# Optimization experiments

Hardware: AMD Instinct MI355X
Metric: run time of the kernel (lower is better)

The kernel has to match this reference:

```python
import jax, jax.numpy as jnp
import numpy as np

B, S, H = 2, 2048, 1024
NH, G = 16, 4
HD = H // NH          # 64
HPG = NH // G         # 4 heads per kv group


def _xavier(key, fan_in, fan_out):
    limit = np.sqrt(6.0 / (fan_in + fan_out)).astype(np.float32)
    return jax.random.uniform(key, (fan_in, fan_out), jnp.float32, -limit, limit)


def setup_inputs() -> dict:
    key = jax.random.key(0)
    ks = jax.random.split(key, 6)
    hidden_state = jax.random.normal(ks[0], (B, S, H), jnp.float32)
    causal = jnp.tril(jnp.ones((S, S), dtype=bool))
    attention_mask = jnp.broadcast_to(causal, (B, NH, S, S))
    # weights stored as (in, out); torch nn.Linear computes x @ W.T, equivalent math
    Wq = _xavier(ks[1], H, H)
    Wk = _xavier(ks[2], H, G * HD)
    Wv = _xavier(ks[3], H, G * HD)
    Wo = _xavier(ks[4], H, H)
    bq = jnp.zeros((H,), jnp.float32)
    bk = jnp.zeros((G * HD,), jnp.float32)
    bv = jnp.zeros((G * HD,), jnp.float32)
    bo = jnp.zeros((H,), jnp.float32)
    return {"hidden_state": hidden_state, "attention_mask": attention_mask,
            "Wq": Wq, "bq": bq, "Wk": Wk, "bk": bk,
            "Wv": Wv, "bv": bv, "Wo": Wo, "bo": bo}


def reference(hidden_state, attention_mask, Wq, bq, Wk, bk, Wv, bv, Wo, bo):
    b, s, _ = hidden_state.shape
    scale = jnp.float32(1.0 / np.sqrt(HD))
    # projections; query heads split as (group, head_in_group) = head-major order
    q = (hidden_state @ Wq + bq).reshape(b, s, G, HPG, HD)
    k = (hidden_state @ Wk + bk).reshape(b, s, G, HD)
    v = (hidden_state @ Wv + bv).reshape(b, s, G, HD)
    # scores: [b, G, HPG, S, S]  (kv broadcast over heads_per_group, as in torch expand)
    scores = jnp.einsum('bqghd,bkgd->bghqk', q, k) * scale
    mask = attention_mask.reshape(b, G, HPG, s, s)
    scores = jnp.where(mask, scores, -jnp.inf)
    w = jax.nn.softmax(scores, axis=-1)  # dropout=0 (eval): identity
    out = jnp.einsum('bghqk,bkgd->bqghd', w, v).reshape(b, s, H)
    return out @ Wo + bo
```

## Files before the change

### kernel.cpp

```cpp
#include <hip/hip_runtime.h>

#define BATCH 2
#define SEQ   2048
#define HDIM  1024
#define NHEAD 16
#define NGRP  4
#define HDHD  64
#define QKVN  1536
#define MROWS (BATCH*SEQ)

#define DI __device__ __forceinline__

typedef __attribute__((ext_vector_type(4))) float f32x4;
typedef __attribute__((ext_vector_type(8))) __bf16 bf16x8;
typedef __attribute__((ext_vector_type(8))) unsigned short ushort8;

DI unsigned short f2bf(float f) {
    unsigned int u = __float_as_uint(f);
    u += 0x7FFF + ((u >> 16) & 1);
    return (unsigned short)(u >> 16);
}

DI void async16(const void* g, void* l) {
    __builtin_amdgcn_global_load_lds(
        (const __attribute__((address_space(1))) unsigned int*)g,
        (__attribute__((address_space(3))) unsigned int*)l, 16, 0, 0);
}

#define MFMA16(a, b, c) __builtin_amdgcn_mfma_f32_16x16x32_bf16((a), (b), (c), 0, 0, 0)

__global__ __launch_bounds__(256) void cvt_bf16_kernel(
    const float* __restrict__ in, unsigned short* __restrict__ out, int n8)
{
    int i = blockIdx.x * 256 + threadIdx.x;
    if (i >= n8) return;
    const float4* p = (const float4*)in;
    float4 a = p[i * 2];
    float4 b = p[i * 2 + 1];
    ushort8 r;
    r[0] = f2bf(a.x); r[1] = f2bf(a.y); r[2] = f2bf(a.z); r[3] = f2bf(a.w);
    r[4] = f2bf(b.x); r[5] = f2bf(b.y); r[6] = f2bf(b.z); r[7] = f2bf(b.w);
    *(ushort8*)&out[i * 8] = r;
}

__global__ __launch_bounds__(256) void wtrans_kernel(
    const float* __restrict__ W, unsigned short* __restrict__ Wt, int K, int N)
{
    __shared__ float t[32][33];
    int k0 = blockIdx.y * 32, n0 = blockIdx.x * 32;
    int tx = threadIdx.x & 31, ty = threadIdx.x >> 5;
#pragma unroll
    for (int i = 0; i < 4; ++i)
        t[ty + i * 8][tx] = W[(size_t)(k0 + ty + i * 8) * N + n0 + tx];
    __syncthreads();
#pragma unroll
    for (int i = 0; i < 4; ++i)
        Wt[(size_t)(n0 + ty + i * 8) * K + k0 + tx] = f2bf(t[tx][ty + i * 8]);
}

__global__ void biascat_kernel(const float* __restrict__ bq,
                               const float* __restrict__ bk,
                               const float* __restrict__ bv,
                               float* __restrict__ out)
{
    int i = blockIdx.x * 256 + threadIdx.x;
    if (i < 1024)      out[i] = bq[i];
    else if (i < 1280) out[i] = bk[i - 1024];
    else if (i < 1536) out[i] = bv[i - 1280];
}

template<bool BF16_OUT>
__global__ __launch_bounds__(256) void gemm_bt(
    const unsigned short* __restrict__ A,
    const unsigned short* __restrict__ Bt,
    const float* __restrict__ bias,
    void* __restrict__ C,
    int M, int N, int K, int ldc)
{
    __shared__ unsigned short Asm[128 * 64];
    __shared__ unsigned short Bsm[128 * 64];
    const int tid = threadIdx.x;
    const int lane = tid & 63;
    const int w = tid >> 6;
    const int l15 = lane & 15;
    const int l4  = lane >> 4;
    const int m0 = blockIdx.y * 128;
    const int n0 = blockIdx.x * 128;
    const int wm = (w >> 1) * 64;
    const int wn = (w & 1) * 64;

    f32x4 acc[4][4] = {};

    const int srow = tid >> 3;
    const int c8   = (tid & 7) * 8;

    for (int kb = 0; kb < K; kb += 64) {
#pragma unroll
        for (int i = 0; i < 4; ++i) {
            int r = srow + i * 32;
            async16(&A[(size_t)(m0 + r) * K + kb + c8], &Asm[r * 64 + c8]);
        }
#pragma unroll
        for (int i = 0; i < 4; ++i) {
            int r = srow + i * 32;
            async16(&Bt[(size_t)(n0 + r) * K + kb + c8], &Bsm[r * 64 + c8]);
        }
        __syncthreads();
#pragma unroll
        for (int kk = 0; kk < 2; ++kk) {
            bf16x8 a[4], b[4];
#pragma unroll
            for (int mi = 0; mi < 4; ++mi)
                a[mi] = *(const bf16x8*)&Asm[(wm + mi * 16 + l15) * 64 + kk * 32 + l4 * 8];
#pragma unroll
            for (int ni = 0; ni < 4; ++ni)
                b[ni] = *(const bf16x8*)&Bsm[(wn + ni * 16 + l15) * 64 + kk * 32 + l4 * 8];
#pragma unroll
            for (int mi = 0; mi < 4; ++mi)
#pragma unroll
                for (int ni = 0; ni < 4; ++ni)
                    acc[mi][ni] = MFMA16(a[mi], b[ni], acc[mi][ni]);
        }
        __syncthreads();
    }

#pragma unroll
    for (int ni = 0; ni < 4; ++ni) {
        int n = n0 + wn + ni * 16 + l15;
        float bv = bias[n];
#pragma unroll
        for (int mi = 0; mi < 4; ++mi) {
            int mrow = m0 + wm + mi * 16 + l4 * 4;
#pragma unroll
            for (int r = 0; r < 4; ++r) {
                float v = acc[mi][ni][r] + bv;
                if (BF16_OUT)
                    ((unsigned short*)C)[(size_t)(mrow + r) * ldc + n] = f2bf(v);
                else
                    ((float*)C)[(size_t)(mrow + r) * ldc + n] = v;
            }
        }
    }
}

__global__ __launch_bounds__(256) void vtrans_kernel(
    const unsigned short* __restrict__ QKV, unsigned short* __restrict__ Vt)
{
    int bg = blockIdx.y;
    int s0 = blockIdx.x * 64;
    int b = bg >> 2, g = bg & 3;
    int t = threadIdx.x;
    int sr = t >> 3;
    int dc = (t & 7) * 8;
#pragma unroll
    for (int p = 0; p < 2; ++p) {
        int s = s0 + sr + p * 32;
        ushort8 v = *(const ushort8*)&QKV[(size_t)(b * SEQ + s) * QKVN + 1280 + g * 64 + dc];
#pragma unroll
        for (int j = 0; j < 8; ++j)
            Vt[((size_t)bg * 64 + dc + j) * SEQ + s] = v[j];
    }
}

__global__ __launch_bounds__(256) void flash_gqa(
    const unsigned short* __restrict__ QKV,
    const unsigned short* __restrict__ Vt,
    unsigned short* __restrict__ O)
{
    const int tid  = threadIdx.x;
    const int lane = tid & 63;
    const int w    = tid >> 6;
    const int l15  = lane & 15;
    const int l4   = lane >> 4;
    const int qb   = blockIdx.x;
    const int h    = blockIdx.y;
    const int b    = blockIdx.z;
    const int g    = h >> 2;
    const int q0   = qb * 64 + w * 16;

    __shared__ unsigned short Pl[4][16 * 72];
    unsigned short* P = &Pl[w][0];

    const unsigned short* Qb = QKV + (size_t)(b * SEQ) * QKVN + h * 64;
    const unsigned short* Kb = QKV + (size_t)(b * SEQ) * QKVN + 1024 + g * 64;
    const unsigned short* Vb = Vt + ((size_t)(b * NGRP + g) * 64) * SEQ;

    bf16x8 qa[2];
#pragma unroll
    for (int ks = 0; ks < 2; ++ks)
        qa[ks] = *(const bf16x8*)&Qb[(size_t)(q0 + l15) * QKVN + ks * 32 + l4 * 8];

    f32x4 acc[4] = {};
    float m[4], ssum[4];
#pragma unroll
    for (int r = 0; r < 4; ++r) { m[r] = -1e30f; ssum[r] = 0.f; }

    const float scale = 0.125f;
    const int nkt = qb + 1;

    for (int kt = 0; kt < nkt; ++kt) {
        const int kbase = kt * 64;
        f32x4 st[4];
#pragma unroll
        for (int n = 0; n < 4; ++n) {
            f32x4 s4 = {0.f, 0.f, 0.f, 0.f};
#pragma unroll
            for (int ks = 0; ks < 2; ++ks) {
                bf16x8 kf = *(const bf16x8*)&Kb[(size_t)(kbase + n * 16 + l15) * QKVN + ks * 32 + l4 * 8];
                s4 = MFMA16(qa[ks], kf, s4);
            }
            st[n] = s4;
        }
        const bool diag = (kbase + 63 > q0);
#pragma unroll
        for (int n = 0; n < 4; ++n)
#pragma unroll
            for (int r = 0; r < 4; ++r) {
                float v = st[n][r] * scale;
                if (diag) {
                    int key = kbase + n * 16 + l15;
                    int q   = q0 + l4 * 4 + r;
                    if (key > q) v = -1e30f;
                }
                st[n][r] = v;
            }
        float tm[4];
#pragma unroll
        for (int r = 0; r < 4; ++r)
            tm[r] = fmaxf(fmaxf(st[0][r], st[1][r]), fmaxf(st[2][r], st[3][r]));
#pragma unroll
        for (int msk = 1; msk < 16; msk <<= 1)
#pragma unroll
            for (int r = 0; r < 4; ++r)
                tm[r] = fmaxf(tm[r], __shfl_xor(tm[r], msk, 64));
        float fr[4];
#pragma unroll
        for (int r = 0; r < 4; ++r) {
            float mn = fmaxf(m[r], tm[r]);
            fr[r] = __expf(m[r] - mn);
            m[r] = mn;
        }
        float rs[4] = {0.f, 0.f, 0.f, 0.f};
#pragma unroll
        for (int n = 0; n < 4; ++n)
#pragma unroll
            for (int r = 0; r < 4; ++r) {
                float p = __expf(st[n][r] - m[r]);
                st[n][r] = p;
                rs[r] += p;
            }
#pragma unroll
        for (int msk = 1; msk < 16; msk <<= 1)
#pragma unroll
            for (int r = 0; r < 4; ++r)
                rs[r] += __shfl_xor(rs[r], msk, 64);
#pragma unroll
        for (int r = 0; r < 4; ++r) ssum[r] = ssum[r] * fr[r] + rs[r];
#pragma unroll
        for (int n = 0; n < 4; ++n)
#pragma unroll
            for (int r = 0; r < 4; ++r) acc[n][r] *= fr[r];
#pragma unroll
        for (int n = 0; n < 4; ++n)
#pragma unroll
            for (int r = 0; r < 4; ++r)
                P[(l4 * 4 + r) * 72 + n * 16 + l15] = f2bf(st[n][r]);
        __syncthreads();
#pragma unroll
        for (int n = 0; n < 4; ++n) {
#pragma unroll
            for (int ks = 0; ks < 2; ++ks) {
                bf16x8 pa = *(const bf16x8*)&P[l15 * 72 + ks * 32 + l4 * 8];
                bf16x8 vb = *(const bf16x8*)&Vb[(size_t)(n * 16 + l15) * SEQ + kbase + ks * 32 + l4 * 8];
                acc[n] = MFMA16(pa, vb, acc[n]);
            }
        }
        __syncthreads();
    }

    float inv[4];
#pragma unroll
    for (int r = 0; r < 4; ++r) inv[r] = 1.f / ssum[r];
#pragma unroll
    for (int n = 0; n < 4; ++n)
#pragma unroll
        for (int r = 0; r < 4; ++r) {
            float v = acc[n][r] * inv[r];
            O[(size_t)(b * SEQ + q0 + l4 * 4 + r) * HDIM + h * 64 + n * 16 + l15] = f2bf(v);
        }
}

extern "C" void kernel_launch(void* const* d_in, const int* in_sizes, int n_in,
                              void* d_out, int out_size, void* d_ws, size_t ws_size,
                              hipStream_t stream)
{
    const float* hidden = (const float*)d_in[0];
    const float* Wq = (const float*)d_in[2];
    const float* bq = (const float*)d_in[3];
    const float* Wk = (const float*)d_in[4];
    const float* bk = (const float*)d_in[5];
    const float* Wv = (const float*)d_in[6];
    const float* bv = (const float*)d_in[7];
    const float* Wo = (const float*)d_in[8];
    const float* bo = (const float*)d_in[9];

    char* ws = (char*)d_ws;
    unsigned short* Xb      = (unsigned short*)(ws);
    unsigned short* QKV     = (unsigned short*)(ws + 8388608);
    unsigned short* WqkvT   = (unsigned short*)(ws + 20971520);
    unsigned short* WoT     = (unsigned short*)(ws + 24117248);
    unsigned short* Vt      = (unsigned short*)(ws + 26214400);
    unsigned short* AttnOut = (unsigned short*)(ws + 30408704);
    float*          bqkv    = (float*)(ws + 38797312);

    cvt_bf16_kernel<<<dim3((MROWS * HDIM) / 8 / 256), 256, 0, stream>>>(hidden, Xb, (MROWS * HDIM) / 8);

    wtrans_kernel<<<dim3(32, 32), 256, 0, stream>>>(Wq, WqkvT,                  HDIM, 1024);
    wtrans_kernel<<<dim3( 8, 32), 256, 0, stream>>>(Wk, WqkvT + 1024 * HDIM,    HDIM,  256);
    wtrans_kernel<<<dim3( 8, 32), 256, 0, stream>>>(Wv, WqkvT + 1280 * HDIM,    HDIM,  256);
    wtrans_kernel<<<dim3(32, 32), 256, 0, stream>>>(Wo, WoT,                    HDIM, 1024);

    biascat_kernel<<<dim3(6), 256, 0, stream>>>(bq, bk, bv, bqkv);

    gemm_bt<true><<<dim3(QKVN / 128, MROWS / 128), 256, 0, stream>>>(
        Xb, WqkvT, bqkv, QKV, MROWS, QKVN, HDIM, QKVN);

    vtrans_kernel<<<dim3(SEQ / 64, BATCH * NGRP), 256, 0, stream>>>(QKV, Vt);

    flash_gqa<<<dim3(SEQ / 64, NHEAD, BATCH), 256, 0, stream>>>(QKV, Vt, AttnOut);

    gemm_bt<false><<<dim3(HDIM / 128, MROWS / 128), 256, 0, stream>>>(
        AttnOut, WoT, bo, (float*)d_out, MROWS, HDIM, HDIM, HDIM);
}
```

Measured before the change: 944.6 us.

## Pre-pack K/V into MFMA fragment layouts in QKV GEMM epilogue; drop LDS P staging

The QKV GEMM epilogue now writes K and V directly into fragment-packed layouts, so the separate V transpose kernel is no longer needed and flash attention reads K and V with contiguous 16-byte loads instead of strided row reads. The attention kernel computes S transposed (K as the A operand), which lets the exponentiated probabilities be packed straight into bf16 A fragments for the PV MFMA without the shared-memory round trip and the two block barriers per tile. It also folds the scale into an exp2 constant and computes row sums with an MFMA against a ones vector instead of shuffle reductions. The cost is more complex scattered epilogue stores in the projection GEMM and an extra cross-lane shuffle to broadcast the rescale factors.

```diff
diff --git a/kernel.cpp b/kernel.cpp
--- a/kernel.cpp
+++ b/kernel.cpp
@@ -5,7 +5,6 @@
 #define HDIM  1024
 #define NHEAD 16
 #define NGRP  4
-#define HDHD  64
 #define QKVN  1536
 #define MROWS (BATCH*SEQ)
 
@@ -14,12 +13,15 @@
 typedef __attribute__((ext_vector_type(4))) float f32x4;
 typedef __attribute__((ext_vector_type(8))) __bf16 bf16x8;
 typedef __attribute__((ext_vector_type(8))) unsigned short ushort8;
+typedef __attribute__((ext_vector_type(4))) unsigned short us4;
 
 DI unsigned short f2bf(float f) {
     unsigned int u = __float_as_uint(f);
     u += 0x7FFF + ((u >> 16) & 1);
     return (unsigned short)(u >> 16);
 }
+
+DI bf16x8 u2b(ushort8 u) { union { ushort8 u; bf16x8 b; } x; x.u = u; return x.b; }
 
 DI void async16(const void* g, void* l) {
     __builtin_amdgcn_global_load_lds(
@@ -69,12 +71,14 @@
     else if (i < 1536) out[i] = bv[i - 1280];
 }
 
-template<bool BF16_OUT>
+template<int MODE>
 __global__ __launch_bounds__(256) void gemm_bt(
     const unsigned short* __restrict__ A,
     const unsigned short* __restrict__ Bt,
     const float* __restrict__ bias,
     void* __restrict__ C,
+    unsigned short* __restrict__ Kp,
+    unsigned short* __restrict__ Vp,
     int M, int N, int K, int ldc)
 {
     __shared__ unsigned short Asm[128 * 64];
@@ -124,47 +128,70 @@
         __syncthreads();
     }
 
-#pragma unroll
-    for (int ni = 0; ni < 4; ++ni) {
-        int n = n0 + wn + ni * 16 + l15;
-        float bv = bias[n];
-#pragma unroll
-        for (int mi = 0; mi < 4; ++mi) {
-            int mrow = m0 + wm + mi * 16 + l4 * 4;
-#pragma unroll
-            for (int r = 0; r < 4; ++r) {
-                float v = acc[mi][ni][r] + bv;
-                if (BF16_OUT)
-                    ((unsigned short*)C)[(size_t)(mrow + r) * ldc + n] = f2bf(v);
-                else
-                    ((float*)C)[(size_t)(mrow + r) * ldc + n] = v;
-            }
-        }
-    }
-}
-
-__global__ __launch_bounds__(256) void vtrans_kernel(
-    const unsigned short* __restrict__ QKV, unsigned short* __restrict__ Vt)
-{
-    int bg = blockIdx.y;
-    int s0 = blockIdx.x * 64;
-    int b = bg >> 2, g = bg & 3;
-    int t = threadIdx.x;
-    int sr = t >> 3;
-    int dc = (t & 7) * 8;
-#pragma unroll
-    for (int p = 0; p < 2; ++p) {
-        int s = s0 + sr + p * 32;
-        ushort8 v = *(const ushort8*)&QKV[(size_t)(b * SEQ + s) * QKVN + 1280 + g * 64 + dc];
-#pragma unroll
-        for (int j = 0; j < 8; ++j)
-            Vt[((size_t)bg * 64 + dc + j) * SEQ + s] = v[j];
+    if (MODE == 0) {
+#pragma unroll
+        for (int ni = 0; ni < 4; ++ni) {
+            int n = n0 + wn + ni * 16 + l15;
+            float bv = bias[n];
+#pragma unroll
+            for (int mi = 0; mi < 4; ++mi) {
+                int mrow = m0 + wm + mi * 16 + l4 * 4;
+#pragma unroll
+                for (int r = 0; r < 4; ++r)
+                    ((float*)C)[(size_t)(mrow + r) * ldc + n] = acc[mi][ni][r] + bv;
+            }
+        }
+    } else {
+        const int bidx = m0 >> 11;
+#pragma unroll
+        for (int ni = 0; ni < 4; ++ni) {
+            const int nb = n0 + wn + ni * 16;
+            const float bv = bias[nb + l15];
+            if (nb < 1024) {
+#pragma unroll
+                for (int mi = 0; mi < 4; ++mi) {
+                    int mrow = m0 + wm + mi * 16 + l4 * 4;
+#pragma unroll
+                    for (int r = 0; r < 4; ++r)
+                        ((unsigned short*)C)[(size_t)(mrow + r) * ldc + nb + l15] =
+                            f2bf(acc[mi][ni][r] + bv);
+                }
+            } else if (nb < 1280) {
+                const int g  = (nb - 1024) >> 6;
+                const int d  = ((nb - 1024) & 63) + l15;
+                unsigned short* Kb = Kp + (size_t)(bidx * NGRP + g) * 131072
+                                        + (d >> 5) * 512 + (d & 31);
+#pragma unroll
+                for (int mi = 0; mi < 4; ++mi) {
+                    int mrow = m0 + wm + mi * 16 + l4 * 4;
+#pragma unroll
+                    for (int r = 0; r < 4; ++r) {
+                        int s = (mrow + r) & 2047;
+                        Kb[(s >> 4) * 1024 + (s & 15) * 32] = f2bf(acc[mi][ni][r] + bv);
+                    }
+                }
+            } else {
+                const int g = (nb - 1280) >> 6;
+                const int d = ((nb - 1280) & 63) + l15;
+                unsigned short* Vb = Vp + (size_t)(bidx * NGRP + g) * 131072 + d * 32;
+#pragma unroll
+                for (int mi = 0; mi < 4; ++mi) {
+                    int srow = (m0 + wm + mi * 16 + l4 * 4) & 2047;
+                    us4 u;
+#pragma unroll
+                    for (int r = 0; r < 4; ++r) u[r] = f2bf(acc[mi][ni][r] + bv);
+                    int pos = (((srow & 15) >> 2) * 8) + (((srow >> 4) & 1) * 4);
+                    *(us4*)&Vb[(srow >> 5) * 2048 + pos] = u;
+                }
+            }
+        }
     }
 }
 
 __global__ __launch_bounds__(256) void flash_gqa(
     const unsigned short* __restrict__ QKV,
-    const unsigned short* __restrict__ Vt,
+    const unsigned short* __restrict__ Kp,
+    const unsigned short* __restrict__ Vp,
     unsigned short* __restrict__ O)
 {
     const int tid  = threadIdx.x;
@@ -177,117 +204,106 @@
     const int b    = blockIdx.z;
     const int g    = h >> 2;
     const int q0   = qb * 64 + w * 16;
-
-    __shared__ unsigned short Pl[4][16 * 72];
-    unsigned short* P = &Pl[w][0];
+    const int q    = q0 + l15;
 
     const unsigned short* Qb = QKV + (size_t)(b * SEQ) * QKVN + h * 64;
-    const unsigned short* Kb = QKV + (size_t)(b * SEQ) * QKVN + 1024 + g * 64;
-    const unsigned short* Vb = Vt + ((size_t)(b * NGRP + g) * 64) * SEQ;
-
-    bf16x8 qa[2];
+    const unsigned short* Kb = Kp + (size_t)(b * NGRP + g) * 131072;
+    const unsigned short* Vb = Vp + (size_t)(b * NGRP + g) * 131072;
+
+    bf16x8 qf[2];
 #pragma unroll
     for (int ks = 0; ks < 2; ++ks)
-        qa[ks] = *(const bf16x8*)&Qb[(size_t)(q0 + l15) * QKVN + ks * 32 + l4 * 8];
+        qf[ks] = *(const bf16x8*)&Qb[(size_t)(q0 + l15) * QKVN + ks * 32 + l4 * 8];
+
+    ushort8 ou;
+#pragma unroll
+    for (int j = 0; j < 8; ++j) ou[j] = 0x3F80;
+    const bf16x8 ones = u2b(ou);
 
     f32x4 acc[4] = {};
-    float m[4], ssum[4];
-#pragma unroll
-    for (int r = 0; r < 4; ++r) { m[r] = -1e30f; ssum[r] = 0.f; }
-
-    const float scale = 0.125f;
+    f32x4 ssum = {0.f, 0.f, 0.f, 0.f};
+    float m = -1e30f;
+    const float SCL = 0.18033688f;
     const int nkt = qb + 1;
 
     for (int kt = 0; kt < nkt; ++kt) {
         const int kbase = kt * 64;
+        const unsigned short* Kt = Kb + (size_t)(kt * 4) * 1024;
         f32x4 st[4];
 #pragma unroll
+        for (int t = 0; t < 4; ++t) {
+            f32x4 s4 = {0.f, 0.f, 0.f, 0.f};
+#pragma unroll
+            for (int ks = 0; ks < 2; ++ks) {
+                bf16x8 kf = *(const bf16x8*)&Kt[t * 1024 + ks * 512 + l15 * 32 + l4 * 8];
+                s4 = MFMA16(kf, qf[ks], s4);
+            }
+            st[t] = s4;
+        }
+        const bool diag = (kbase + 63 > q0);
+#pragma unroll
+        for (int t = 0; t < 4; ++t)
+#pragma unroll
+            for (int r = 0; r < 4; ++r) {
+                float v = st[t][r] * SCL;
+                if (diag && (kbase + t * 16 + l4 * 4 + r > q)) v = -1e30f;
+                st[t][r] = v;
+            }
+        float tm = st[0][0];
+#pragma unroll
+        for (int t = 0; t < 4; ++t)
+#pragma unroll
+            for (int r = 0; r < 4; ++r) tm = fmaxf(tm, st[t][r]);
+        tm = fmaxf(tm, __shfl_xor(tm, 16, 64));
+        tm = fmaxf(tm, __shfl_xor(tm, 32, 64));
+        const float mn = fmaxf(m, tm);
+        const float fr = __builtin_amdgcn_exp2f(m - mn);
+        m = mn;
+#pragma unroll
+        for (int t = 0; t < 4; ++t)
+#pragma unroll
+            for (int r = 0; r < 4; ++r)
+                st[t][r] = __builtin_amdgcn_exp2f(st[t][r] - mn);
+        bf16x8 pa0, pa1;
+#pragma unroll
+        for (int r = 0; r < 4; ++r) {
+            pa0[r]     = (__bf16)st[0][r];
+            pa0[4 + r] = (__bf16)st[1][r];
+            pa1[r]     = (__bf16)st[2][r];
+            pa1[4 + r] = (__bf16)st[3][r];
+        }
+        f32x4 frr;
+#pragma unroll
+        for (int r = 0; r < 4; ++r) frr[r] = __shfl(fr, l4 * 4 + r, 64);
+#pragma unroll
+        for (int n = 0; n < 4; ++n)
+#pragma unroll
+            for (int r = 0; r < 4; ++r) acc[n][r] *= frr[r];
+        f32x4 rs = {0.f, 0.f, 0.f, 0.f};
+        rs = MFMA16(pa0, ones, rs);
+        rs = MFMA16(pa1, ones, rs);
+#pragma unroll
+        for (int r = 0; r < 4; ++r) ssum[r] = ssum[r] * frr[r] + rs[r];
+        const unsigned short* Vt0 = Vb + (size_t)(kt * 2) * 2048;
+#pragma unroll
         for (int n = 0; n < 4; ++n) {
-            f32x4 s4 = {0.f, 0.f, 0.f, 0.f};
-#pragma unroll
-            for (int ks = 0; ks < 2; ++ks) {
-                bf16x8 kf = *(const bf16x8*)&Kb[(size_t)(kbase + n * 16 + l15) * QKVN + ks * 32 + l4 * 8];
-                s4 = MFMA16(qa[ks], kf, s4);
-            }
-            st[n] = s4;
-        }
-        const bool diag = (kbase + 63 > q0);
-#pragma unroll
-        for (int n = 0; n < 4; ++n)
-#pragma unroll
-            for (int r = 0; r < 4; ++r) {
-                float v = st[n][r] * scale;
-                if (diag) {
-                    int key = kbase + n * 16 + l15;
-                    int q   = q0 + l4 * 4 + r;
-                    if (key > q) v = -1e30f;
-                }
-                st[n][r] = v;
-            }
-        float tm[4];
+#pragma unroll
+            for (int s2 = 0; s2 < 2; ++s2) {
+                bf16x8 vf = *(const bf16x8*)&Vt0[s2 * 2048 + (n * 16 + l15) * 32 + l4 * 8];
+                acc[n] = MFMA16(s2 ? pa1 : pa0, vf, acc[n]);
+            }
+        }
+    }
+
+    f32x4 inv;
+#pragma unroll
+    for (int r = 0; r < 4; ++r) inv[r] = 1.f / ssum[r];
+#pragma unroll
+    for (int n = 0; n < 4; ++n)
 #pragma unroll
         for (int r = 0; r < 4; ++r)
-            tm[r] = fmaxf(fmaxf(st[0][r], st[1][r]), fmaxf(st[2][r], st[3][r]));
-#pragma unroll
-        for (int msk = 1; msk < 16; msk <<= 1)
-#pragma unroll
-            for (int r = 0; r < 4; ++r)
-                tm[r] = fmaxf(tm[r], __shfl_xor(tm[r], msk, 64));
-        float fr[4];
-#pragma unroll
-        for (int r = 0; r < 4; ++r) {
-            float mn = fmaxf(m[r], tm[r]);
-            fr[r] = __expf(m[r] - mn);
-            m[r] = mn;
-        }
-        float rs[4] = {0.f, 0.f, 0.f, 0.f};
-#pragma unroll
-        for (int n = 0; n < 4; ++n)
-#pragma unroll
-            for (int r = 0; r < 4; ++r) {
-                float p = __expf(st[n][r] - m[r]);
-                st[n][r] = p;
-                rs[r] += p;
-            }
-#pragma unroll
-        for (int msk = 1; msk < 16; msk <<= 1)
-#pragma unroll
-            for (int r = 0; r < 4; ++r)
-                rs[r] += __shfl_xor(rs[r], msk, 64);
-#pragma unroll
-        for (int r = 0; r < 4; ++r) ssum[r] = ssum[r] * fr[r] + rs[r];
-#pragma unroll
-        for (int n = 0; n < 4; ++n)
-#pragma unroll
-            for (int r = 0; r < 4; ++r) acc[n][r] *= fr[r];
-#pragma unroll
-        for (int n = 0; n < 4; ++n)
-#pragma unroll
-            for (int r = 0; r < 4; ++r)
-                P[(l4 * 4 + r) * 72 + n * 16 + l15] = f2bf(st[n][r]);
-        __syncthreads();
-#pragma unroll
-        for (int n = 0; n < 4; ++n) {
-#pragma unroll
-            for (int ks = 0; ks < 2; ++ks) {
-                bf16x8 pa = *(const bf16x8*)&P[l15 * 72 + ks * 32 + l4 * 8];
-                bf16x8 vb = *(const bf16x8*)&Vb[(size_t)(n * 16 + l15) * SEQ + kbase + ks * 32 + l4 * 8];
-                acc[n] = MFMA16(pa, vb, acc[n]);
-            }
-        }
-        __syncthreads();
-    }
-
-    float inv[4];
-#pragma unroll
-    for (int r = 0; r < 4; ++r) inv[r] = 1.f / ssum[r];
-#pragma unroll
-    for (int n = 0; n < 4; ++n)
-#pragma unroll
-        for (int r = 0; r < 4; ++r) {
-            float v = acc[n][r] * inv[r];
-            O[(size_t)(b * SEQ + q0 + l4 * 4 + r) * HDIM + h * 64 + n * 16 + l15] = f2bf(v);
-        }
+            O[(size_t)(b * SEQ + q0 + l4 * 4 + r) * HDIM + h * 64 + n * 16 + l15] =
+                f2bf(acc[n][r] * inv[r]);
 }
 
 extern "C" void kernel_launch(void* const* d_in, const int* in_sizes, int n_in,
@@ -309,26 +325,25 @@
     unsigned short* QKV     = (unsigned short*)(ws + 8388608);
     unsigned short* WqkvT   = (unsigned short*)(ws + 20971520);
     unsigned short* WoT     = (unsigned short*)(ws + 24117248);
-    unsigned short* Vt      = (unsigned short*)(ws + 26214400);
+    unsigned short* Kp      = (unsigned short*)(ws + 26214400);
+    unsigned short* Vp      = (unsigned short*)(ws + 28311552);
     unsigned short* AttnOut = (unsigned short*)(ws + 30408704);
     float*          bqkv    = (float*)(ws + 38797312);
 
     cvt_bf16_kernel<<<dim3((MROWS * HDIM) / 8 / 256), 256, 0, stream>>>(hidden, Xb, (MROWS * HDIM) / 8);
 
-    wtrans_kernel<<<dim3(32, 32), 256, 0, stream>>>(Wq, WqkvT,                  HDIM, 1024);
-    wtrans_kernel<<<dim3( 8, 32), 256, 0, stream>>>(Wk, WqkvT + 1024 * HDIM,    HDIM,  256);
-    wtrans_kernel<<<dim3( 8, 32), 256, 0, stream>>>(Wv, WqkvT + 1280 * HDIM,    HDIM,  256);
-    wtrans_kernel<<<dim3(32, 32), 256, 0, stream>>>(Wo, WoT,                    HDIM, 1024);
+    wtrans_kernel<<<dim3(32, 32), 256, 0, stream>>>(Wq, WqkvT,               HDIM, 1024);
+    wtrans_kernel<<<dim3( 8, 32), 256, 0, stream>>>(Wk, WqkvT + 1024 * HDIM, HDIM,  256);
+    wtrans_kernel<<<dim3( 8, 32), 256, 0, stream>>>(Wv, WqkvT + 1280 * HDIM, HDIM,  256);
+    wtrans_kernel<<<dim3(32, 32), 256, 0, stream>>>(Wo, WoT,                 HDIM, 1024);
 
     biascat_kernel<<<dim3(6), 256, 0, stream>>>(bq, bk, bv, bqkv);
 
-    gemm_bt<true><<<dim3(QKVN / 128, MROWS / 128), 256, 0, stream>>>(
-        Xb, WqkvT, bqkv, QKV, MROWS, QKVN, HDIM, QKVN);
-
-    vtrans_kernel<<<dim3(SEQ / 64, BATCH * NGRP), 256, 0, stream>>>(QKV, Vt);
-
-    flash_gqa<<<dim3(SEQ / 64, NHEAD, BATCH), 256, 0, stream>>>(QKV, Vt, AttnOut);
-
-    gemm_bt<false><<<dim3(HDIM / 128, MROWS / 128), 256, 0, stream>>>(
-        AttnOut, WoT, bo, (float*)d_out, MROWS, HDIM, HDIM, HDIM);
-}
+    gemm_bt<1><<<dim3(QKVN / 128, MROWS / 128), 256, 0, stream>>>(
+        Xb, WqkvT, bqkv, QKV, Kp, Vp, MROWS, QKVN, HDIM, QKVN);
+
+    flash_gqa<<<dim3(SEQ / 64, NHEAD, BATCH), 256, 0, stream>>>(QKV, Kp, Vp, AttnOut);
+
+    gemm_bt<0><<<dim3(HDIM / 128, MROWS / 128), 256, 0, stream>>>(
+        AttnOut, WoT, bo, (float*)d_out, nullptr, nullptr, MROWS, HDIM, HDIM, HDIM);
+}
```

Measured after the change: 772.3 us. -18.2%, faster.
